# Kernel optimization log

Hardware: AMD Instinct MI355X
Metric: run time of the kernel (lower is better)

The kernel has to match this reference:

```python
import jax, jax.numpy as jnp
import numpy as np

CUTOFF = 5.2
BOX = 60.0  # Angstrom bounding box edge


def setup_inputs() -> dict:
    key = jax.random.key(0)
    k1, _ = jax.random.split(key)
    N = 6144
    coordinates = jax.random.uniform(k1, (1, N, 3), dtype=jnp.float32) * BOX
    species = jnp.zeros((1, N), dtype=jnp.int32)  # no dummy (-1) atoms
    return {"species": species, "coordinates": coordinates}


def reference(species, coordinates):
    # CellList.forward with cell=None, pbc=None: bucketing is only an
    # acceleration structure; the math is: all unordered atom pairs with
    # distance <= cutoff, dummy atoms (species == -1) excluded.
    # Fixed-shape jit-compatible form: all i<j pairs + in_cutoff mask.
    N = coordinates.shape[1]
    i, j = jnp.triu_indices(N, k=1)              # P = N(N-1)/2 static pairs
    coords = coordinates.reshape(-1, 3)
    dummy = species.reshape(-1) == -1
    valid = ~(dummy[i] | dummy[j])

    # screening distances use detached coordinates (as in _screen_with_cutoff)
    cdet = jax.lax.stop_gradient(coords)
    diff_det = cdet[i] - cdet[j]                 # [P, 3]
    dist_det = jnp.sqrt(jnp.sum(diff_det * diff_det, axis=-1))
    in_cutoff = (dist_det <= CUTOFF) & valid     # [P] bool

    # recompute diff/dist with differentiable coords on surviving pairs
    raw_diff = coords[i] - coords[j]
    diff = raw_diff * in_cutoff[:, None].astype(raw_diff.dtype)
    sq = jnp.sum(raw_diff * raw_diff, axis=-1)
    safe_sq = jnp.where(in_cutoff, sq, 1.0)      # avoid sqrt(0) grad NaN
    dist = jnp.where(in_cutoff, jnp.sqrt(safe_sq), 0.0)

    atom_pairs = jnp.stack([i, j])               # [2, P]
    return atom_pairs, in_cutoff, diff, dist
```

## Files before the change

### kernel.cpp

```cpp
#include <hip/hip_runtime.h>


__global__ __launch_bounds__(256) void cell_pairs_f32(
    const int* __restrict__ species,
    const float* __restrict__ coords,
    float* __restrict__ out,
    int N, int P)
{
    __shared__ float ldsd[3072];

    const int t   = threadIdx.x;
    const int blk = blockIdx.x << 10;
    if (blk >= P) return;
    const bool full = (blk + 1024 <= P);
    const int twoNm1 = 2 * N - 1;
    const size_t Ps = (size_t)P;

    if (full) {
#pragma unroll
        for (int k = 0; k < 4; ++k) {
            const int p = blk + (k << 8) + t;

            long long disc_i = (long long)twoNm1 * (long long)twoNm1
                             - 8LL * (long long)p;
            float sr = __fsqrt_rn((float)disc_i);
            int i = (int)(((float)twoNm1 - sr) * 0.5f);
            if (i < 0) i = 0;
            if (i > N - 2) i = N - 2;
            long long ri = ((long long)i * (long long)(twoNm1 - i)) >> 1;
            while (i < N - 2) {
                long long rn = ((long long)(i + 1) * (long long)(twoNm1 - (i + 1))) >> 1;
                if (rn <= (long long)p) { ++i; ri = rn; } else break;
            }
            while (i > 0 && ri > (long long)p) {
                --i; ri = ((long long)i * (long long)(twoNm1 - i)) >> 1;
            }
            const int j = i + 1 + (int)((long long)p - ri);

            float dx = coords[3 * i + 0] - coords[3 * j + 0];
            float dy = coords[3 * i + 1] - coords[3 * j + 1];
            float dz = coords[3 * i + 2] - coords[3 * j + 2];
            float sq = __fadd_rn(__fadd_rn(__fmul_rn(dx, dx), __fmul_rn(dy, dy)),
                                 __fmul_rn(dz, dz));
            float d  = __fsqrt_rn(sq);
            bool inc = (d <= 5.2f) && (species[i] != -1) && (species[j] != -1);
            float m  = inc ? 1.0f : 0.0f;

            out[(size_t)p]          = (float)i;
            out[Ps + (size_t)p]     = (float)j;
            out[2 * Ps + (size_t)p] = m;
            out[6 * Ps + (size_t)p] = __fmul_rn(d, m);

            const int q = (k << 8) + t;
            ldsd[3 * q + 0] = __fmul_rn(dx, m);
            ldsd[3 * q + 1] = __fmul_rn(dy, m);
            ldsd[3 * q + 2] = __fmul_rn(dz, m);
        }

        __syncthreads();

        const float4* lr = reinterpret_cast<const float4*>(ldsd);
        float4 d0 = lr[t];
        float4 d1 = lr[t + 256];
        float4 d2 = lr[t + 512];
        float* gd = out + 3 * Ps + 3 * (size_t)blk;
        reinterpret_cast<float4*>(gd)[t]        = d0;
        reinterpret_cast<float4*>(gd + 1024)[t] = d1;
        reinterpret_cast<float4*>(gd + 2048)[t] = d2;
    } else {
        for (int k = 0; k < 4; ++k) {
            const int p = blk + (k << 8) + t;
            if (p >= P) continue;
            long long disc_i = (long long)twoNm1 * (long long)twoNm1
                             - 8LL * (long long)p;
            float sr = __fsqrt_rn((float)disc_i);
            int i = (int)(((float)twoNm1 - sr) * 0.5f);
            if (i < 0) i = 0;
            if (i > N - 2) i = N - 2;
            long long ri = ((long long)i * (long long)(twoNm1 - i)) >> 1;
            while (i < N - 2) {
                long long rn = ((long long)(i + 1) * (long long)(twoNm1 - (i + 1))) >> 1;
                if (rn <= (long long)p) { ++i; ri = rn; } else break;
            }
            while (i > 0 && ri > (long long)p) {
                --i; ri = ((long long)i * (long long)(twoNm1 - i)) >> 1;
            }
            const int j = i + 1 + (int)((long long)p - ri);

            float dx = coords[3 * i + 0] - coords[3 * j + 0];
            float dy = coords[3 * i + 1] - coords[3 * j + 1];
            float dz = coords[3 * i + 2] - coords[3 * j + 2];
            float sq = __fadd_rn(__fadd_rn(__fmul_rn(dx, dx), __fmul_rn(dy, dy)),
                                 __fmul_rn(dz, dz));
            float d  = __fsqrt_rn(sq);
            bool inc = (d <= 5.2f) && (species[i] != -1) && (species[j] != -1);
            float m  = inc ? 1.0f : 0.0f;

            size_t pp = (size_t)p;
            out[pp]                  = (float)i;
            out[Ps + pp]             = (float)j;
            out[2 * Ps + pp]         = m;
            out[3 * Ps + 3 * pp + 0] = __fmul_rn(dx, m);
            out[3 * Ps + 3 * pp + 1] = __fmul_rn(dy, m);
            out[3 * Ps + 3 * pp + 2] = __fmul_rn(dz, m);
            out[6 * Ps + pp]         = __fmul_rn(d, m);
        }
    }
}

extern "C" void kernel_launch(void* const* d_in, const int* in_sizes, int n_in,
                              void* d_out, int out_size, void* d_ws, size_t ws_size,
                              hipStream_t stream) {
    const int*   species = (const int*)d_in[0];
    const float* coords  = (const float*)d_in[1];
    int N = in_sizes[0];
    long long Pll = (long long)N * (long long)(N - 1) / 2;
    int P = (int)Pll;

    long long blocks = (Pll + 1023) >> 10;
    cell_pairs_f32<<<dim3((unsigned)blocks), dim3(256), 0, stream>>>(
        species, coords, (float*)d_out, N, P);
}
```

Measured before the change: 102.4 us.

## Split fused pair kernel into per-output kernels with grid-stride loops

Replaces the single kernel that wrote all seven output streams with five kernels, one per output region (i, j, mask, diff, dist). Each kernel uses a grid-stride loop over 1024-pair tiles on a grid capped at 2048 blocks. The likely aim is to keep each kernel writing only one contiguous stream, which may improve DRAM write locality. In exchange every kernel recomputes the index decode, and three of them redo the coordinate gather and distance, while also adding launch overhead.

```diff
diff --git a/kernel.cpp b/kernel.cpp
--- a/kernel.cpp
+++ b/kernel.cpp
@@ -1,109 +1,122 @@
 #include <hip/hip_runtime.h>
 
 
-__global__ __launch_bounds__(256) void cell_pairs_f32(
-    const int* __restrict__ species,
-    const float* __restrict__ coords,
-    float* __restrict__ out,
-    int N, int P)
-{
-    __shared__ float ldsd[3072];
+static __device__ __forceinline__ void decode_ij(int p, int N, int twoNm1,
+                                                 int& io, int& jo) {
+    long long disc_i = (long long)twoNm1 * (long long)twoNm1 - 8LL * (long long)p;
+    float sr = __fsqrt_rn((float)disc_i);
+    int i = (int)(((float)twoNm1 - sr) * 0.5f);
+    if (i < 0) i = 0;
+    if (i > N - 2) i = N - 2;
+    long long ri = ((long long)i * (long long)(twoNm1 - i)) >> 1;
+    while (i < N - 2) {
+        long long rn = ((long long)(i + 1) * (long long)(twoNm1 - (i + 1))) >> 1;
+        if (rn <= (long long)p) { ++i; ri = rn; } else break;
+    }
+    while (i > 0 && ri > (long long)p) {
+        --i; ri = ((long long)i * (long long)(twoNm1 - i)) >> 1;
+    }
+    io = i;
+    jo = i + 1 + (int)((long long)p - ri);
+}
 
-    const int t   = threadIdx.x;
-    const int blk = blockIdx.x << 10;
-    if (blk >= P) return;
-    const bool full = (blk + 1024 <= P);
+static __device__ __forceinline__ float geom(const int* species,
+                                             const float* coords, int i, int j,
+                                             float& dx, float& dy, float& dz,
+                                             float& d) {
+    dx = coords[3 * i + 0] - coords[3 * j + 0];
+    dy = coords[3 * i + 1] - coords[3 * j + 1];
+    dz = coords[3 * i + 2] - coords[3 * j + 2];
+    float sq = __fadd_rn(__fadd_rn(__fmul_rn(dx, dx), __fmul_rn(dy, dy)),
+                         __fmul_rn(dz, dz));
+    d = __fsqrt_rn(sq);
+    bool inc = (d <= 5.2f) && (species[i] != -1) && (species[j] != -1);
+    return inc ? 1.0f : 0.0f;
+}
+
+template <int WHICH>
+__global__ __launch_bounds__(256) void k_idx(float* __restrict__ dst,
+                                             int N, int P, int ntiles) {
+    const int t = threadIdx.x;
     const int twoNm1 = 2 * N - 1;
-    const size_t Ps = (size_t)P;
-
-    if (full) {
+    for (int tile = blockIdx.x; tile < ntiles; tile += gridDim.x) {
+        const int base = tile << 10;
 #pragma unroll
         for (int k = 0; k < 4; ++k) {
-            const int p = blk + (k << 8) + t;
+            const int p = base + (k << 8) + t;
+            if (p < P) {
+                int i, j; decode_ij(p, N, twoNm1, i, j);
+                dst[p] = WHICH ? (float)j : (float)i;
+            }
+        }
+    }
+}
 
-            long long disc_i = (long long)twoNm1 * (long long)twoNm1
-                             - 8LL * (long long)p;
-            float sr = __fsqrt_rn((float)disc_i);
-            int i = (int)(((float)twoNm1 - sr) * 0.5f);
-            if (i < 0) i = 0;
-            if (i > N - 2) i = N - 2;
-            long long ri = ((long long)i * (long long)(twoNm1 - i)) >> 1;
-            while (i < N - 2) {
-                long long rn = ((long long)(i + 1) * (long long)(twoNm1 - (i + 1))) >> 1;
-                if (rn <= (long long)p) { ++i; ri = rn; } else break;
+template <int MODE>
+__global__ __launch_bounds__(256) void k_geo(const int* __restrict__ species,
+                                             const float* __restrict__ coords,
+                                             float* __restrict__ dst,
+                                             int N, int P, int ntiles) {
+    const int t = threadIdx.x;
+    const int twoNm1 = 2 * N - 1;
+    for (int tile = blockIdx.x; tile < ntiles; tile += gridDim.x) {
+        const int base = tile << 10;
+#pragma unroll
+        for (int k = 0; k < 4; ++k) {
+            const int p = base + (k << 8) + t;
+            if (p < P) {
+                int i, j; decode_ij(p, N, twoNm1, i, j);
+                float dx, dy, dz, d;
+                float m = geom(species, coords, i, j, dx, dy, dz, d);
+                dst[p] = MODE ? __fmul_rn(d, m) : m;
             }
-            while (i > 0 && ri > (long long)p) {
-                --i; ri = ((long long)i * (long long)(twoNm1 - i)) >> 1;
+        }
+    }
+}
+
+__global__ __launch_bounds__(256) void k_diff(const int* __restrict__ species,
+                                              const float* __restrict__ coords,
+                                              float* __restrict__ dst,
+                                              int N, int P, int ntiles) {
+    __shared__ float ldsd[3072];
+    const int t = threadIdx.x;
+    const int twoNm1 = 2 * N - 1;
+    for (int tile = blockIdx.x; tile < ntiles; tile += gridDim.x) {
+        const int base = tile << 10;
+        const bool full = (base + 1024 <= P);
+        if (full) {
+#pragma unroll
+            for (int k = 0; k < 4; ++k) {
+                const int p = base + (k << 8) + t;
+                int i, j; decode_ij(p, N, twoNm1, i, j);
+                float dx, dy, dz, d;
+                float m = geom(species, coords, i, j, dx, dy, dz, d);
+                const int q = (k << 8) + t;
+                ldsd[3 * q + 0] = __fmul_rn(dx, m);
+                ldsd[3 * q + 1] = __fmul_rn(dy, m);
+                ldsd[3 * q + 2] = __fmul_rn(dz, m);
             }
-            const int j = i + 1 + (int)((long long)p - ri);
-
-            float dx = coords[3 * i + 0] - coords[3 * j + 0];
-            float dy = coords[3 * i + 1] - coords[3 * j + 1];
-            float dz = coords[3 * i + 2] - coords[3 * j + 2];
-            float sq = __fadd_rn(__fadd_rn(__fmul_rn(dx, dx), __fmul_rn(dy, dy)),
-                                 __fmul_rn(dz, dz));
-            float d  = __fsqrt_rn(sq);
-            bool inc = (d <= 5.2f) && (species[i] != -1) && (species[j] != -1);
-            float m  = inc ? 1.0f : 0.0f;
-
-            out[(size_t)p]          = (float)i;
-            out[Ps + (size_t)p]     = (float)j;
-            out[2 * Ps + (size_t)p] = m;
-            out[6 * Ps + (size_t)p] = __fmul_rn(d, m);
-
-            const int q = (k << 8) + t;
-            ldsd[3 * q + 0] = __fmul_rn(dx, m);
-            ldsd[3 * q + 1] = __fmul_rn(dy, m);
-            ldsd[3 * q + 2] = __fmul_rn(dz, m);
-        }
-
-        __syncthreads();
-
-        const float4* lr = reinterpret_cast<const float4*>(ldsd);
-        float4 d0 = lr[t];
-        float4 d1 = lr[t + 256];
-        float4 d2 = lr[t + 512];
-        float* gd = out + 3 * Ps + 3 * (size_t)blk;
-        reinterpret_cast<float4*>(gd)[t]        = d0;
-        reinterpret_cast<float4*>(gd + 1024)[t] = d1;
-        reinterpret_cast<float4*>(gd + 2048)[t] = d2;
-    } else {
-        for (int k = 0; k < 4; ++k) {
-            const int p = blk + (k << 8) + t;
-            if (p >= P) continue;
-            long long disc_i = (long long)twoNm1 * (long long)twoNm1
-                             - 8LL * (long long)p;
-            float sr = __fsqrt_rn((float)disc_i);
-            int i = (int)(((float)twoNm1 - sr) * 0.5f);
-            if (i < 0) i = 0;
-            if (i > N - 2) i = N - 2;
-            long long ri = ((long long)i * (long long)(twoNm1 - i)) >> 1;
-            while (i < N - 2) {
-                long long rn = ((long long)(i + 1) * (long long)(twoNm1 - (i + 1))) >> 1;
-                if (rn <= (long long)p) { ++i; ri = rn; } else break;
+            __syncthreads();
+            const float4* lr = reinterpret_cast<const float4*>(ldsd);
+            float4 d0 = lr[t];
+            float4 d1 = lr[t + 256];
+            float4 d2 = lr[t + 512];
+            float* gd = dst + 3 * (size_t)base;
+            reinterpret_cast<float4*>(gd)[t]        = d0;
+            reinterpret_cast<float4*>(gd + 1024)[t] = d1;
+            reinterpret_cast<float4*>(gd + 2048)[t] = d2;
+            __syncthreads();
+        } else {
+            for (int k = 0; k < 4; ++k) {
+                const int p = base + (k << 8) + t;
+                if (p >= P) continue;
+                int i, j; decode_ij(p, N, twoNm1, i, j);
+                float dx, dy, dz, d;
+                float m = geom(species, coords, i, j, dx, dy, dz, d);
+                dst[3 * (size_t)p + 0] = __fmul_rn(dx, m);
+                dst[3 * (size_t)p + 1] = __fmul_rn(dy, m);
+                dst[3 * (size_t)p + 2] = __fmul_rn(dz, m);
             }
-            while (i > 0 && ri > (long long)p) {
-                --i; ri = ((long long)i * (long long)(twoNm1 - i)) >> 1;
-            }
-            const int j = i + 1 + (int)((long long)p - ri);
-
-            float dx = coords[3 * i + 0] - coords[3 * j + 0];
-            float dy = coords[3 * i + 1] - coords[3 * j + 1];
-            float dz = coords[3 * i + 2] - coords[3 * j + 2];
-            float sq = __fadd_rn(__fadd_rn(__fmul_rn(dx, dx), __fmul_rn(dy, dy)),
-                                 __fmul_rn(dz, dz));
-            float d  = __fsqrt_rn(sq);
-            bool inc = (d <= 5.2f) && (species[i] != -1) && (species[j] != -1);
-            float m  = inc ? 1.0f : 0.0f;
-
-            size_t pp = (size_t)p;
-            out[pp]                  = (float)i;
-            out[Ps + pp]             = (float)j;
-            out[2 * Ps + pp]         = m;
-            out[3 * Ps + 3 * pp + 0] = __fmul_rn(dx, m);
-            out[3 * Ps + 3 * pp + 1] = __fmul_rn(dy, m);
-            out[3 * Ps + 3 * pp + 2] = __fmul_rn(dz, m);
-            out[6 * Ps + pp]         = __fmul_rn(d, m);
         }
     }
 }
@@ -113,11 +126,20 @@
                               hipStream_t stream) {
     const int*   species = (const int*)d_in[0];
     const float* coords  = (const float*)d_in[1];
+    float*       out     = (float*)d_out;
     int N = in_sizes[0];
     long long Pll = (long long)N * (long long)(N - 1) / 2;
     int P = (int)Pll;
+    size_t Ps = (size_t)P;
 
-    long long blocks = (Pll + 1023) >> 10;
-    cell_pairs_f32<<<dim3((unsigned)blocks), dim3(256), 0, stream>>>(
-        species, coords, (float*)d_out, N, P);
+    int ntiles = (int)((Pll + 1023) >> 10);
+    int grid = 2048;
+    if (grid > ntiles) grid = ntiles;
+    dim3 g((unsigned)grid), b(256);
+
+    k_idx<0><<<g, b, 0, stream>>>(out,          N, P, ntiles);
+    k_idx<1><<<g, b, 0, stream>>>(out + Ps,     N, P, ntiles);
+    k_geo<0><<<g, b, 0, stream>>>(species, coords, out + 2 * Ps, N, P, ntiles);
+    k_diff  <<<g, b, 0, stream>>>(species, coords, out + 3 * Ps, N, P, ntiles);
+    k_geo<1><<<g, b, 0, stream>>>(species, coords, out + 6 * Ps, N, P, ntiles);
 }
```

Measured after the change: 200.3 us. 1.96x slower.
